# Performance work log

Hardware: AMD Instinct MI355X
Metric: run time of the kernel (lower is better)

Reference implementation:

```python
import jax, jax.numpy as jnp
import numpy as np

TG22 = 0.4142135623730951  # tan(22.5 deg)
TG67 = 2.414213562373095   # tan(67.5 deg)


def _canny(gray):
    # gray: [B,H,W] float in [0,255]; cv2 path casts to uint8 -> truncate
    g = jnp.floor(jnp.clip(gray, 0.0, 255.0))
    p = jnp.pad(g, ((0, 0), (1, 1), (1, 1)), mode='edge')  # BORDER_REPLICATE
    # Sobel 3x3 (cross-correlation) via shifted slices
    gx = (p[:, :-2, 2:] + 2.0 * p[:, 1:-1, 2:] + p[:, 2:, 2:]
          - p[:, :-2, :-2] - 2.0 * p[:, 1:-1, :-2] - p[:, 2:, :-2])
    gy = (p[:, 2:, :-2] + 2.0 * p[:, 2:, 1:-1] + p[:, 2:, 2:]
          - p[:, :-2, :-2] - 2.0 * p[:, :-2, 1:-1] - p[:, :-2, 2:])
    mag = jnp.abs(gx) + jnp.abs(gy)  # cv2.Canny default L1 gradient
    # 8 neighbors of magnitude (zero-padded)
    pm = jnp.pad(mag, ((0, 0), (1, 1), (1, 1)))
    e = pm[:, 1:-1, 2:]; w = pm[:, 1:-1, :-2]
    n = pm[:, :-2, 1:-1]; s = pm[:, 2:, 1:-1]
    nw = pm[:, :-2, :-2]; se = pm[:, 2:, 2:]
    ne = pm[:, :-2, 2:]; sw = pm[:, 2:, :-2]
    # quantize gradient direction into 4 bins and do non-max suppression
    ax, ay = jnp.abs(gx), jnp.abs(gy)
    horiz = ay <= TG22 * ax          # gradient ~horizontal -> compare E/W
    vert = ay > TG67 * ax            # gradient ~vertical   -> compare N/S
    same_sign = (gx * gy) >= 0.0     # 45-deg diagonal choice
    n1 = jnp.where(horiz, e, jnp.where(vert, n, jnp.where(same_sign, nw, ne)))
    n2 = jnp.where(horiz, w, jnp.where(vert, s, jnp.where(same_sign, se, sw)))
    keep = (mag > n1) & (mag >= n2)
    nms = jnp.where(keep, mag, 0.0)
    strong = nms > 150.0
    weak = nms > 50.0

    def dilate3x3(m):
        mp = jnp.pad(m, ((0, 0), (1, 1), (1, 1)))
        H, W_ = m.shape[1], m.shape[2]
        acc = m
        for di in (0, 1, 2):
            for dj in (0, 1, 2):
                acc = acc | mp[:, di:di + H, dj:dj + W_]
        return acc

    # hysteresis: grow strong into connected weak pixels until fixed point
    def cond(st):
        prev, cur = st
        return jnp.any(prev != cur)

    def body(st):
        _, cur = st
        nxt = cur | (weak & dilate3x3(cur))
        return (cur, nxt)

    _, final = jax.lax.while_loop(cond, body, (jnp.zeros_like(strong), strong))
    return final.astype(jnp.float32) * 255.0  # cv2.Canny outputs 0/255


def setup_inputs() -> dict:
    key = jax.random.key(0)
    k1, k2, k3 = jax.random.split(key, 3)
    B, C, H, W_ = 16, 3, 512, 512
    OC = 32
    x = jax.random.uniform(k1, (B, C, H, W_), dtype=jnp.float32) * 255.0
    W = jax.random.normal(k2, (OC, C + 1), dtype=jnp.float32) * (1.0 / np.sqrt(C + 1))
    b = jax.random.normal(k3, (OC,), dtype=jnp.float32) * 0.01
    return {"x": x, "W": W, "b": b}


def reference(x, W, b):
    # grayscale
    gray = 0.2989 * x[:, 0] + 0.587 * x[:, 1] + 0.114 * x[:, 2]  # [B,H,W]
    # edge branch is detached in the original (cpu().detach())
    edge = jax.lax.stop_gradient(_canny(gray))[:, None]  # [B,1,H,W]
    cat = jnp.concatenate([x, edge], axis=1)  # [B,4,H,W]
    out = jnp.einsum('bchw,oc->bohw', cat, W) + b[None, :, None, None]
    return jax.nn.relu(out)
```

## Files before the change

### kernel.cpp

```cpp
#include <hip/hip_runtime.h>
#include <stdint.h>

typedef unsigned long long u64;
typedef float __attribute__((ext_vector_type(4))) fvec4;

#define MD_OFF   (4ull << 20)
#define WK_OFF   (12ull << 20)
#define ST_OFF   ((12ull << 20) + (512ull << 10))
#define ED_OFF   ((12ull << 20) + (1024ull << 10))

__global__ __launch_bounds__(256) void k_gray(const float* __restrict__ x,
                                              unsigned char* __restrict__ g) {
#pragma clang fp contract(off)
    const float C0 = (float)0.2989, C1 = (float)0.587, C2 = (float)0.114;
    int i   = blockIdx.x * 256 + threadIdx.x;
    int b   = i >> 16;
    int rem = i & 65535;
    const float* xb = x + (size_t)b * 786432 + (size_t)rem * 4;
    float4 r0 = *(const float4*)(xb);
    float4 r1 = *(const float4*)(xb + 262144);
    float4 r2 = *(const float4*)(xb + 524288);
    float g0 = C0 * r0.x + C1 * r1.x + C2 * r2.x;
    float g1 = C0 * r0.y + C1 * r1.y + C2 * r2.y;
    float g2 = C0 * r0.z + C1 * r1.z + C2 * r2.z;
    float g3 = C0 * r0.w + C1 * r1.w + C2 * r2.w;
    g0 = floorf(fminf(fmaxf(g0, 0.0f), 255.0f));
    g1 = floorf(fminf(fmaxf(g1, 0.0f), 255.0f));
    g2 = floorf(fminf(fmaxf(g2, 0.0f), 255.0f));
    g3 = floorf(fminf(fmaxf(g3, 0.0f), 255.0f));
    uchar4 st = make_uchar4((unsigned char)g0, (unsigned char)g1,
                            (unsigned char)g2, (unsigned char)g3);
    *(uchar4*)(g + (size_t)b * 262144 + (size_t)rem * 4) = st;
}

__global__ __launch_bounds__(256) void k_sobel(const unsigned char* __restrict__ g,
                                               unsigned short* __restrict__ magdir) {
    const float TG22f = (float)0.4142135623730951;
    const float TG67f = (float)2.414213562373095;
    int i = blockIdx.x * 256 + threadIdx.x;
    int b = i >> 18;
    int r = (i >> 9) & 511;
    int w = i & 511;
    const unsigned char* gb = g + (size_t)b * 262144;
    int rm = r > 0 ? r - 1 : 0, rp = r < 511 ? r + 1 : 511;
    int wm = w > 0 ? w - 1 : 0, wp = w < 511 ? w + 1 : 511;
    int a00 = gb[rm * 512 + wm], a01 = gb[rm * 512 + w], a02 = gb[rm * 512 + wp];
    int a10 = gb[r  * 512 + wm],                          a12 = gb[r  * 512 + wp];
    int a20 = gb[rp * 512 + wm], a21 = gb[rp * 512 + w],  a22 = gb[rp * 512 + wp];
    int gx = a02 + 2 * a12 + a22 - a00 - 2 * a10 - a20;
    int gy = a20 + 2 * a21 + a22 - a00 - 2 * a01 - a02;
    int ax = gx < 0 ? -gx : gx;
    int ay = gy < 0 ? -gy : gy;
    int mag = ax + ay;
    float fax = (float)ax, fay = (float)ay;
    unsigned dir;
    if (fay <= TG22f * fax)      dir = 0u;
    else if (fay > TG67f * fax)  dir = 1u;
    else                         dir = (gx * gy >= 0) ? 2u : 3u;
    magdir[i] = (unsigned short)(mag | (dir << 12));
}

__global__ __launch_bounds__(256) void k_nms(const unsigned short* __restrict__ magdir,
                                             u64* __restrict__ weakw,
                                             u64* __restrict__ strongw) {
    int i = blockIdx.x * 256 + threadIdx.x;
    int b = i >> 18;
    int r = (i >> 9) & 511;
    int w = i & 511;
    const unsigned short* mb = magdir + (size_t)b * 262144;
    int md  = mb[r * 512 + w];
    int mag = md & 0x7FF;
    int dir = md >> 12;
    auto ldm = [&](int rr, int ww) -> int {
        if ((unsigned)rr > 511u || (unsigned)ww > 511u) return 0;
        return (int)(mb[rr * 512 + ww] & 0x7FF);
    };
    int n1, n2;
    if (dir == 0)      { n1 = ldm(r, w + 1);     n2 = ldm(r, w - 1); }
    else if (dir == 1) { n1 = ldm(r - 1, w);     n2 = ldm(r + 1, w); }
    else if (dir == 2) { n1 = ldm(r - 1, w - 1); n2 = ldm(r + 1, w + 1); }
    else               { n1 = ldm(r - 1, w + 1); n2 = ldm(r + 1, w - 1); }
    bool keep = (mag > n1) && (mag >= n2);
    int nms = keep ? mag : 0;
    u64 wb = __ballot(nms > 50);
    u64 sb = __ballot(nms > 150);
    int widx = ((b << 9) + r) * 8 + (w >> 6);
    int lane = threadIdx.x & 63;
    if (lane == 0) weakw[widx]   = wb;
    else if (lane == 1) strongw[widx] = sb;
}

__device__ inline u64 upfill(u64 w, u64 s) {
    return ((((w + s) ^ w) & w) | s);
}
__device__ inline u64 runfill(u64 w, u64 s) {
    u64 u = upfill(w, s);
    u64 d = __brevll(upfill(__brevll(w), __brevll(s)));
    return u | d;
}

#define HST 9

__global__ __launch_bounds__(1024) void k_hyst(const u64* __restrict__ weakg,
                                               const u64* __restrict__ strongg,
                                               u64* __restrict__ edgeg) {
    __shared__ u64 sc[512 * HST];
    __shared__ int sflag;
    int b = blockIdx.x;
    int t = threadIdx.x;
    const u64* wk = weakg + (size_t)b * 4096;
    const u64* st = strongg + (size_t)b * 4096;
#pragma unroll
    for (int i = 0; i < 4; ++i) {
        int ig = i * 1024 + t;
        int r = ig >> 3, c = ig & 7;
        sc[r * HST + c] = st[ig];
    }
    int c  = t & 7;
    int r0 = (t >> 3) * 4;
    u64 wreg[4];
#pragma unroll
    for (int j = 0; j < 4; ++j) wreg[j] = wk[(r0 + j) * 8 + c];
    if (t == 0) sflag = 0;
    const bool hasL = c > 0, hasR = c < 7;
    __syncthreads();

    for (;;) {
        bool ch = false;
        {
            u64 carry = (r0 > 0) ? sc[(r0 - 1) * HST + c] : 0;
#pragma unroll
            for (int j = 0; j < 4; ++j) {
                int r = r0 + j;
                int idx = r * HST + c;
                u64 wv = wreg[j];
                u64 self = sc[idx];
                if (self == wv) { carry = self; continue; }
                u64 dm = (r < 511) ? sc[idx + HST] : 0;
                u64 lor = 0, ror_ = 0;
                if (hasL) {
                    u64 lm = sc[idx - 1];
                    u64 lu = (r > 0)   ? sc[idx - HST - 1] : 0;
                    u64 ld = (r < 511) ? sc[idx + HST - 1] : 0;
                    lor = lm | lu | ld;
                }
                if (hasR) {
                    u64 rm = sc[idx + 1];
                    u64 ru = (r > 0)   ? sc[idx - HST + 1] : 0;
                    u64 rd = (r < 511) ? sc[idx + HST + 1] : 0;
                    ror_ = rm | ru | rd;
                }
                u64 vert = carry | dm | self;
                u64 dil = vert | (vert << 1) | (vert >> 1)
                        | (lor >> 63) | (ror_ << 63);
                u64 nv = runfill(wv, self | (wv & dil));
                if (nv != self) { sc[idx] = nv; ch = true; }
                carry = nv;
            }
        }
        {
            u64 carry = (r0 + 4 < 512) ? sc[(r0 + 4) * HST + c] : 0;
#pragma unroll
            for (int j = 3; j >= 0; --j) {
                int r = r0 + j;
                int idx = r * HST + c;
                u64 wv = wreg[j];
                u64 self = sc[idx];
                if (self == wv) { carry = self; continue; }
                u64 um = (r > 0) ? sc[idx - HST] : 0;
                u64 lor = 0, ror_ = 0;
                if (hasL) {
                    u64 lm = sc[idx - 1];
                    u64 lu = (r > 0)   ? sc[idx - HST - 1] : 0;
                    u64 ld = (r < 511) ? sc[idx + HST - 1] : 0;
                    lor = lm | lu | ld;
                }
                if (hasR) {
                    u64 rm = sc[idx + 1];
                    u64 ru = (r > 0)   ? sc[idx - HST + 1] : 0;
                    u64 rd = (r < 511) ? sc[idx + HST + 1] : 0;
                    ror_ = rm | ru | rd;
                }
                u64 vert = um | carry | self;
                u64 dil = vert | (vert << 1) | (vert >> 1)
                        | (lor >> 63) | (ror_ << 63);
                u64 nv = runfill(wv, self | (wv & dil));
                if (nv != self) { sc[idx] = nv; ch = true; }
                carry = nv;
            }
        }
        if (ch) sflag = 1;
        __syncthreads();
        bool stop = (sflag == 0);
        __syncthreads();
        if (stop) break;
        if (t == 0) sflag = 0;
        __syncthreads();
    }

    u64* eg = edgeg + (size_t)b * 4096;
#pragma unroll
    for (int i = 0; i < 4; ++i) {
        int ig = i * 1024 + t;
        int r = ig >> 3, cc = ig & 7;
        eg[ig] = sc[r * HST + cc];
    }
}

__global__ __launch_bounds__(256) void k_out(const float* __restrict__ x,
                                             const float* __restrict__ Wm,
                                             const float* __restrict__ bv,
                                             const u64* __restrict__ edgeg,
                                             float* __restrict__ out) {
    __shared__ float sW[128];
    __shared__ float sb[32];
    if (threadIdx.x < 128) sW[threadIdx.x] = Wm[threadIdx.x];
    if (threadIdx.x < 32)  sb[threadIdx.x] = bv[threadIdx.x];
    __syncthreads();
    int i   = blockIdx.x * 256 + threadIdx.x;
    int b   = i >> 16;
    int rem = i & 65535;
    size_t pix = (size_t)rem * 4;
    const float* xb = x + (size_t)b * 786432;
    float4 x0 = *(const float4*)(xb + pix);
    float4 x1 = *(const float4*)(xb + 262144 + pix);
    float4 x2 = *(const float4*)(xb + 524288 + pix);
    int r  = rem >> 7;
    int wq = rem & 127;
    u64 ew = edgeg[(((size_t)b * 512 + r) * 8) + (wq >> 4)];
    int sh = (wq & 15) * 4;
    float e0 = ((ew >> (sh + 0)) & 1ull) ? 255.0f : 0.0f;
    float e1 = ((ew >> (sh + 1)) & 1ull) ? 255.0f : 0.0f;
    float e2 = ((ew >> (sh + 2)) & 1ull) ? 255.0f : 0.0f;
    float e3 = ((ew >> (sh + 3)) & 1ull) ? 255.0f : 0.0f;
    float* ob = out + (size_t)b * 32 * 262144 + pix;
#pragma unroll 8
    for (int o = 0; o < 32; ++o) {
        float w0 = sW[o * 4 + 0], w1 = sW[o * 4 + 1];
        float w2 = sW[o * 4 + 2], w3 = sW[o * 4 + 3];
        float bb = sb[o];
        fvec4 v;
        v.x = fmaxf(w0 * x0.x + w1 * x1.x + w2 * x2.x + w3 * e0 + bb, 0.0f);
        v.y = fmaxf(w0 * x0.y + w1 * x1.y + w2 * x2.y + w3 * e1 + bb, 0.0f);
        v.z = fmaxf(w0 * x0.z + w1 * x1.z + w2 * x2.z + w3 * e2 + bb, 0.0f);
        v.w = fmaxf(w0 * x0.w + w1 * x1.w + w2 * x2.w + w3 * e3 + bb, 0.0f);
        __builtin_nontemporal_store(v, (fvec4*)(ob + (size_t)o * 262144));
    }
}

extern "C" void kernel_launch(void* const* d_in, const int* in_sizes, int n_in,
                              void* d_out, int out_size, void* d_ws, size_t ws_size,
                              hipStream_t stream) {
    const float* x  = (const float*)d_in[0];
    const float* Wm = (const float*)d_in[1];
    const float* bv = (const float*)d_in[2];
    float* out = (float*)d_out;
    char* ws = (char*)d_ws;

    unsigned char*  g      = (unsigned char*)(ws);
    unsigned short* magdir = (unsigned short*)(ws + MD_OFF);
    u64* weakw   = (u64*)(ws + WK_OFF);
    u64* strongw = (u64*)(ws + ST_OFF);
    u64* edgew   = (u64*)(ws + ED_OFF);

    k_gray<<<4096, 256, 0, stream>>>(x, g);
    k_sobel<<<16384, 256, 0, stream>>>(g, magdir);
    k_nms<<<16384, 256, 0, stream>>>(magdir, weakw, strongw);
    k_hyst<<<16, 1024, 0, stream>>>(weakw, strongw, edgew);
    k_out<<<4096, 256, 0, stream>>>(x, Wm, bv, edgew, out);
}
```

Measured before the change: 595.8 us.

## Split hysteresis across 256 blocks with grid-wide barriers and halo exchange

Hysteresis used to run as one 1024-thread block per image, so only 16 CUs did the work. It now runs on 256 blocks, 16 row strips per image, each doing one 64-bit word per thread. Each block iterates to a local fixed point in shared memory and publishes its boundary rows to global memory, and a software grid barrier plus a global change counter decide convergence. This spreads the work across many more CUs at the cost of grid barriers per outer round, and it relies on all 256 blocks being co-resident. The barrier and counter words reuse the start of the gray buffer, which has already been consumed by the time k_nms resets them.

```diff
diff --git a/kernel.cpp b/kernel.cpp
--- a/kernel.cpp
+++ b/kernel.cpp
@@ -62,7 +62,12 @@
 
 __global__ __launch_bounds__(256) void k_nms(const unsigned short* __restrict__ magdir,
                                              u64* __restrict__ weakw,
-                                             u64* __restrict__ strongw) {
+                                             u64* __restrict__ strongw,
+                                             unsigned* bar, unsigned* cnt) {
+    if (blockIdx.x == 0 && threadIdx.x == 0) {
+        __hip_atomic_store(bar, 0u, __ATOMIC_RELAXED, __HIP_MEMORY_SCOPE_AGENT);
+        __hip_atomic_store(cnt, 0u, __ATOMIC_RELAXED, __HIP_MEMORY_SCOPE_AGENT);
+    }
     int i = blockIdx.x * 256 + threadIdx.x;
     int b = i >> 18;
     int r = (i >> 9) & 511;
@@ -99,112 +104,90 @@
     return u | d;
 }
 
-#define HST 9
-
-__global__ __launch_bounds__(1024) void k_hyst(const u64* __restrict__ weakg,
+#define HY_GRID 256u
+
+__device__ __forceinline__ void gbar(unsigned* bar, unsigned target) {
+    __syncthreads();
+    if (threadIdx.x == 0) {
+        __threadfence();
+        __hip_atomic_fetch_add(bar, 1u, __ATOMIC_ACQ_REL, __HIP_MEMORY_SCOPE_AGENT);
+        while (__hip_atomic_load(bar, __ATOMIC_ACQUIRE, __HIP_MEMORY_SCOPE_AGENT) < target)
+            __builtin_amdgcn_s_sleep(2);
+        __threadfence();
+    }
+    __syncthreads();
+}
+
+__global__ __launch_bounds__(256) void k_hyst2(const u64* __restrict__ weakg,
                                                const u64* __restrict__ strongg,
-                                               u64* __restrict__ edgeg) {
-    __shared__ u64 sc[512 * HST];
-    __shared__ int sflag;
-    int b = blockIdx.x;
+                                               u64* __restrict__ curg,
+                                               unsigned* bar, unsigned* cnt) {
+    __shared__ u64 sc[34][9];
+    __shared__ unsigned sbc;
+    int blk = blockIdx.x;
+    int b = blk >> 4, s = blk & 15;
     int t = threadIdx.x;
-    const u64* wk = weakg + (size_t)b * 4096;
-    const u64* st = strongg + (size_t)b * 4096;
-#pragma unroll
-    for (int i = 0; i < 4; ++i) {
-        int ig = i * 1024 + t;
-        int r = ig >> 3, c = ig & 7;
-        sc[r * HST + c] = st[ig];
-    }
-    int c  = t & 7;
-    int r0 = (t >> 3) * 4;
-    u64 wreg[4];
-#pragma unroll
-    for (int j = 0; j < 4; ++j) wreg[j] = wk[(r0 + j) * 8 + c];
-    if (t == 0) sflag = 0;
-    const bool hasL = c > 0, hasR = c < 7;
-    __syncthreads();
+    int c = t & 7;
+    int r = t >> 3;
+    int grow = (s << 5) + r;
+    size_t base = (size_t)b * 4096;
+    size_t widx = base + (size_t)grow * 8 + c;
+    u64 wv   = weakg[widx];
+    u64 self = strongg[widx];
+    sc[r + 1][c] = self;
+    bool bdry = (r == 0) || (r == 31);
+    if (bdry)
+        __hip_atomic_store(&curg[widx], self, __ATOMIC_RELEASE, __HIP_MEMORY_SCOPE_AGENT);
+    unsigned ep = 0, prev = 0;
+    ep += 1; gbar(bar, ep * HY_GRID);
 
     for (;;) {
-        bool ch = false;
-        {
-            u64 carry = (r0 > 0) ? sc[(r0 - 1) * HST + c] : 0;
-#pragma unroll
-            for (int j = 0; j < 4; ++j) {
-                int r = r0 + j;
-                int idx = r * HST + c;
-                u64 wv = wreg[j];
-                u64 self = sc[idx];
-                if (self == wv) { carry = self; continue; }
-                u64 dm = (r < 511) ? sc[idx + HST] : 0;
+        if (t < 8) {
+            u64 h = 0;
+            if (s > 0)
+                h = __hip_atomic_load(&curg[base + (size_t)((s << 5) - 1) * 8 + t],
+                                      __ATOMIC_ACQUIRE, __HIP_MEMORY_SCOPE_AGENT);
+            sc[0][t] = h;
+        } else if (t < 16) {
+            u64 h = 0;
+            if (s < 15)
+                h = __hip_atomic_load(&curg[base + (size_t)((s << 5) + 32) * 8 + (t - 8)],
+                                      __ATOMIC_ACQUIRE, __HIP_MEMORY_SCOPE_AGENT);
+            sc[33][t - 8] = h;
+        }
+        __syncthreads();
+        bool bchanged = false;
+        for (;;) {
+            u64 nv = self;
+            if (self != wv) {
+                int rr = r + 1;
+                u64 um = sc[rr - 1][c], dm = sc[rr + 1][c];
                 u64 lor = 0, ror_ = 0;
-                if (hasL) {
-                    u64 lm = sc[idx - 1];
-                    u64 lu = (r > 0)   ? sc[idx - HST - 1] : 0;
-                    u64 ld = (r < 511) ? sc[idx + HST - 1] : 0;
-                    lor = lm | lu | ld;
-                }
-                if (hasR) {
-                    u64 rm = sc[idx + 1];
-                    u64 ru = (r > 0)   ? sc[idx - HST + 1] : 0;
-                    u64 rd = (r < 511) ? sc[idx + HST + 1] : 0;
-                    ror_ = rm | ru | rd;
-                }
-                u64 vert = carry | dm | self;
+                if (c > 0) lor  = sc[rr - 1][c - 1] | sc[rr][c - 1] | sc[rr + 1][c - 1];
+                if (c < 7) ror_ = sc[rr - 1][c + 1] | sc[rr][c + 1] | sc[rr + 1][c + 1];
+                u64 vert = um | dm | self;
                 u64 dil = vert | (vert << 1) | (vert >> 1)
                         | (lor >> 63) | (ror_ << 63);
-                u64 nv = runfill(wv, self | (wv & dil));
-                if (nv != self) { sc[idx] = nv; ch = true; }
-                carry = nv;
+                nv = runfill(wv, self | (wv & dil));
             }
+            bool ch = (nv != self);
+            if (ch) { sc[r + 1][c] = nv; self = nv; }
+            if (!__syncthreads_or((int)ch)) break;
+            bchanged = true;
         }
-        {
-            u64 carry = (r0 + 4 < 512) ? sc[(r0 + 4) * HST + c] : 0;
-#pragma unroll
-            for (int j = 3; j >= 0; --j) {
-                int r = r0 + j;
-                int idx = r * HST + c;
-                u64 wv = wreg[j];
-                u64 self = sc[idx];
-                if (self == wv) { carry = self; continue; }
-                u64 um = (r > 0) ? sc[idx - HST] : 0;
-                u64 lor = 0, ror_ = 0;
-                if (hasL) {
-                    u64 lm = sc[idx - 1];
-                    u64 lu = (r > 0)   ? sc[idx - HST - 1] : 0;
-                    u64 ld = (r < 511) ? sc[idx + HST - 1] : 0;
-                    lor = lm | lu | ld;
-                }
-                if (hasR) {
-                    u64 rm = sc[idx + 1];
-                    u64 ru = (r > 0)   ? sc[idx - HST + 1] : 0;
-                    u64 rd = (r < 511) ? sc[idx + HST + 1] : 0;
-                    ror_ = rm | ru | rd;
-                }
-                u64 vert = um | carry | self;
-                u64 dil = vert | (vert << 1) | (vert >> 1)
-                        | (lor >> 63) | (ror_ << 63);
-                u64 nv = runfill(wv, self | (wv & dil));
-                if (nv != self) { sc[idx] = nv; ch = true; }
-                carry = nv;
-            }
-        }
-        if (ch) sflag = 1;
-        __syncthreads();
-        bool stop = (sflag == 0);
-        __syncthreads();
-        if (stop) break;
-        if (t == 0) sflag = 0;
-        __syncthreads();
-    }
-
-    u64* eg = edgeg + (size_t)b * 4096;
-#pragma unroll
-    for (int i = 0; i < 4; ++i) {
-        int ig = i * 1024 + t;
-        int r = ig >> 3, cc = ig & 7;
-        eg[ig] = sc[r * HST + cc];
-    }
+        if (bdry)
+            __hip_atomic_store(&curg[widx], self, __ATOMIC_RELEASE, __HIP_MEMORY_SCOPE_AGENT);
+        if (t == 0 && bchanged)
+            __hip_atomic_fetch_add(cnt, 1u, __ATOMIC_ACQ_REL, __HIP_MEMORY_SCOPE_AGENT);
+        ep += 1; gbar(bar, ep * HY_GRID);
+        if (t == 0)
+            sbc = __hip_atomic_load(cnt, __ATOMIC_ACQUIRE, __HIP_MEMORY_SCOPE_AGENT);
+        ep += 1; gbar(bar, ep * HY_GRID);
+        unsigned cc = sbc;
+        if (cc == prev) break;
+        prev = cc;
+    }
+    curg[widx] = self;
 }
 
 __global__ __launch_bounds__(256) void k_out(const float* __restrict__ x,
@@ -262,10 +245,12 @@
     u64* weakw   = (u64*)(ws + WK_OFF);
     u64* strongw = (u64*)(ws + ST_OFF);
     u64* edgew   = (u64*)(ws + ED_OFF);
+    unsigned* bar = (unsigned*)(ws);
+    unsigned* cnt = (unsigned*)(ws + 4);
 
     k_gray<<<4096, 256, 0, stream>>>(x, g);
     k_sobel<<<16384, 256, 0, stream>>>(g, magdir);
-    k_nms<<<16384, 256, 0, stream>>>(magdir, weakw, strongw);
-    k_hyst<<<16, 1024, 0, stream>>>(weakw, strongw, edgew);
+    k_nms<<<16384, 256, 0, stream>>>(magdir, weakw, strongw, bar, cnt);
+    k_hyst2<<<(int)HY_GRID, 256, 0, stream>>>(weakw, strongw, edgew, bar, cnt);
     k_out<<<4096, 256, 0, stream>>>(x, Wm, bv, edgew, out);
 }
```

After: 759.5 us. +27.5%, slower.
